# Performance work log

Hardware: AMD Instinct MI355X
Metric: run time of the kernel (lower is better)

## Reference

```python
import jax, jax.numpy as jnp
import numpy as np


def _to_complex(t):
    # last dim 2 = (real, imag) -> complex64
    return jax.lax.complex(t[..., 0], t[..., 1])


def setup_inputs() -> dict:
    key = jax.random.key(0)
    k1, k2, k3, k4 = jax.random.split(key, 4)
    N, C_out, C_in, H, Wf = 2, 64, 3, 256, 129  # Wf = 256//2 + 1 (rfft width)
    X = jax.random.normal(k1, (N, 1, C_in, H, Wf, 2), dtype=jnp.float32)
    D = jax.random.normal(k2, (N, C_out, C_in, H, Wf, 2), dtype=jnp.float32)
    Y = jax.random.normal(k3, (N, C_out, 1, H, Wf, 2), dtype=jnp.float32)
    # alpha is a positive penalty weight; offset away from 0 to avoid blow-up in Z/alpha
    alpha = jax.random.uniform(k4, (N, 1, 1, 1), dtype=jnp.float32) + 0.5
    x_size = np.array([256, 256], dtype=np.int64)  # spatial size for irfft2
    return {"X": X, "D": D, "Y": Y, "alpha": alpha, "x_size": x_size}


def reference(X, D, Y, alpha, x_size):
    C_in = X.shape[2]
    Xc = _to_complex(X)  # (N,1,C_in,H,Wf)
    Dc = _to_complex(D)  # (N,C_out,C_in,H,Wf)
    Yc = _to_complex(Y)  # (N,C_out,1,H,Wf)
    # alpha.unsqueeze(-1).unsqueeze(-1)/C_in: in complex repr one extra axis suffices
    a = (alpha / C_in)[..., None]  # (N,1,1,1,1), real, broadcasts over (N,C_out,C_in,H,Wf)
    Dconj = jnp.conj(Dc)
    Z = Yc * Dc + a * Xc  # (N,C_out,C_in,H,Wf)
    factor1 = Z / a
    numerator = jnp.sum(Dconj * Z, axis=2, keepdims=True)  # (N,C_out,1,H,Wf)
    # csum adds a real scalar (alpha^2) to the real part only
    denominator = a * jnp.sum(Dconj * Dc, axis=2, keepdims=True) + a ** 2
    factor2 = Dc * (numerator / denominator)  # (N,C_out,C_in,H,Wf)
    Xhat = jnp.mean(factor1 - factor2, axis=1)  # (N,C_in,H,Wf)
    Hs, Ws = int(x_size[0]), int(x_size[1])
    # torch.irfft(signal_ndim=2, normalized=False) == full (1/n-normalized) inverse rfft2
    return jnp.fft.irfftn(Xhat, s=(Hs, Ws), axes=(-2, -1))
```

## Files before the change

### kernel.cpp

```cpp
#include <hip/hip_runtime.h>
#include <math.h>

#define H_   256
#define Wf_  129
#define HWf_ 33024
#define CIN_ 3
#define COUT_ 64
#define TW_  0.0245436926f

typedef float f32x4 __attribute__((ext_vector_type(4)));

__global__ __launch_bounds__(256) void solve_stage1(
    const float* __restrict__ X, const float* __restrict__ D,
    const float* __restrict__ Y, const float* __restrict__ alpha,
    float* __restrict__ Xhat)
{
    const int tid  = threadIdx.x;
    const int pl   = tid & 15;
    const int cog  = tid >> 4;
    const int pair = blockIdx.x * 16 + pl;
    const int pos0 = pair * 2;
    const int n    = pos0 / HWf_;
    const int hw0  = pos0 - n * HWf_;

    const float a    = alpha[n] * (1.0f / 3.0f);
    const float inva = 1.0f / a;
    const float a2   = a * a;

    f32x4 x[3];
#pragma unroll
    for (int ci = 0; ci < 3; ++ci)
        x[ci] = *(const f32x4*)(X + ((size_t)(n * 3 + ci) * HWf_ + hw0) * 2);

    const int co0 = cog * 4;
    const float* Dp = D + ((size_t)(n * 64 + co0) * 3) * (HWf_ * 2) + hw0 * 2;
    const float* Yp = Y + ((size_t)(n * 64 + co0)) * (HWf_ * 2) + hw0 * 2;

    float acc[12];
#pragma unroll
    for (int q = 0; q < 12; ++q) acc[q] = 0.f;

#pragma unroll
    for (int co = 0; co < 4; ++co) {
        f32x4 y  = __builtin_nontemporal_load(
                       (const f32x4*)(Yp + (size_t)co * (HWf_ * 2)));
        f32x4 d0 = __builtin_nontemporal_load(
                       (const f32x4*)(Dp + (size_t)(co * 3 + 0) * (HWf_ * 2)));
        f32x4 d1 = __builtin_nontemporal_load(
                       (const f32x4*)(Dp + (size_t)(co * 3 + 1) * (HWf_ * 2)));
        f32x4 d2 = __builtin_nontemporal_load(
                       (const f32x4*)(Dp + (size_t)(co * 3 + 2) * (HWf_ * 2)));

        {
            float s2 = d0[0]*d0[0] + d0[1]*d0[1] + d1[0]*d1[0] + d1[1]*d1[1]
                     + d2[0]*d2[0] + d2[1]*d2[1];
            float sr = d0[0]*x[0][0] + d0[1]*x[0][1] + d1[0]*x[1][0] + d1[1]*x[1][1]
                     + d2[0]*x[2][0] + d2[1]*x[2][1];
            float si = d0[0]*x[0][1] - d0[1]*x[0][0] + d1[0]*x[1][1] - d1[1]*x[1][0]
                     + d2[0]*x[2][1] - d2[1]*x[2][0];
            float nr = y[0] * s2 + a * sr, ni = y[1] * s2 + a * si;
            float invden = 1.0f / (a * s2 + a2);
            float tr = y[0] * inva - nr * invden;
            float ti = y[1] * inva - ni * invden;
            acc[0] += d0[0]*tr - d0[1]*ti;  acc[1] += d0[0]*ti + d0[1]*tr;
            acc[2] += d1[0]*tr - d1[1]*ti;  acc[3] += d1[0]*ti + d1[1]*tr;
            acc[4] += d2[0]*tr - d2[1]*ti;  acc[5] += d2[0]*ti + d2[1]*tr;
        }
        {
            float s2 = d0[2]*d0[2] + d0[3]*d0[3] + d1[2]*d1[2] + d1[3]*d1[3]
                     + d2[2]*d2[2] + d2[3]*d2[3];
            float sr = d0[2]*x[0][2] + d0[3]*x[0][3] + d1[2]*x[1][2] + d1[3]*x[1][3]
                     + d2[2]*x[2][2] + d2[3]*x[2][3];
            float si = d0[2]*x[0][3] - d0[3]*x[0][2] + d1[2]*x[1][3] - d1[3]*x[1][2]
                     + d2[2]*x[2][3] - d2[3]*x[2][2];
            float nr = y[2] * s2 + a * sr, ni = y[3] * s2 + a * si;
            float invden = 1.0f / (a * s2 + a2);
            float tr = y[2] * inva - nr * invden;
            float ti = y[3] * inva - ni * invden;
            acc[6]  += d0[2]*tr - d0[3]*ti;  acc[7]  += d0[2]*ti + d0[3]*tr;
            acc[8]  += d1[2]*tr - d1[3]*ti;  acc[9]  += d1[2]*ti + d1[3]*tr;
            acc[10] += d2[2]*tr - d2[3]*ti;  acc[11] += d2[2]*ti + d2[3]*tr;
        }
    }

    __shared__ float red[16 * 192];
    {
        const int base = cog * 192 + pl * 12;
#pragma unroll
        for (int q = 0; q < 12; ++q) red[base + q] = acc[q];
    }
    __syncthreads();

    if (tid < 192) {
        float s = 0.f;
#pragma unroll
        for (int c = 0; c < 16; ++c) s += red[c * 192 + tid];
        const int P   = tid / 12;
        const int r   = tid - P * 12;
        const int pos = r / 6;
        const int rr  = r - pos * 6;
        const int ci  = rr >> 1;
        const int cc  = rr & 1;
        const int gp  = (blockIdx.x * 16 + P) * 2 + pos;
        const int hw  = gp - n * HWf_;
        const size_t o = ((size_t)(n * 3 + ci) * HWf_ + hw) * 2 + cc;
        Xhat[o] = X[o] + s * (1.0f / 64.0f);
    }
}

__global__ __launch_bounds__(128) void solve_stage2(
    const float2* __restrict__ in, float2* __restrict__ out)
{
    __shared__ float2 col[256];

    const int b    = blockIdx.x;
    const int n_ci = b / Wf_;
    const int w    = b - n_ci * Wf_;
    const int t    = threadIdx.x;

    const float2* src = in + (size_t)n_ci * HWf_ + w;
    col[t]       = src[t * Wf_];
    col[t + 128] = src[(t + 128) * Wf_];
    __syncthreads();

    float wc, wsn;
    sincosf((float)t * TW_, &wsn, &wc);

    float ar = 0.f, ai = 0.f, br = 0.f, bi = 0.f;
    for (int kb = 0; kb < 8; ++kb) {
        const int k0 = kb * 32;
        float tr, ti;
        {
            const int m = (t * k0) & 255;
            float s, c; sincosf((float)m * TW_, &s, &c);
            tr = c; ti = s;
        }
#pragma unroll
        for (int j = 0; j < 32; ++j) {
            const float2 v = col[k0 + j];
            const float pr = v.x * tr - v.y * ti;
            const float pi = v.x * ti + v.y * tr;
            ar += pr; ai += pi;
            if ((k0 + j) & 1) { br -= pr; bi -= pi; }
            else             { br += pr; bi += pi; }
            const float nt = tr * wc - ti * wsn;
            ti = tr * wsn + ti * wc;
            tr = nt;
        }
    }

    float2* dst = out + (size_t)n_ci * HWf_ + w;
    dst[t * Wf_]         = make_float2(ar * (1.0f / 256.0f), ai * (1.0f / 256.0f));
    dst[(t + 128) * Wf_] = make_float2(br * (1.0f / 256.0f), bi * (1.0f / 256.0f));
}

__global__ __launch_bounds__(128) void solve_stage3(
    const float2* __restrict__ in, float* __restrict__ out)
{
    __shared__ float2 row[Wf_];

    const int b = blockIdx.x;
    const int t = threadIdx.x;

    row[t] = in[(size_t)b * Wf_ + t];
    if (t == 0) row[128] = in[(size_t)b * Wf_ + 128];
    __syncthreads();

    float wc, wsn;
    sincosf((float)t * TW_, &wsn, &wc);

    float sa = 0.f, sb = 0.f;
    for (int kb = 0; kb < 4; ++kb) {
        const int k0 = kb * 32;
        float tr, ti;
        {
            const int m = (t * k0) & 255;
            float s, c; sincosf((float)m * TW_, &s, &c);
            tr = c; ti = s;
        }
#pragma unroll
        for (int j = 0; j < 32; ++j) {
            const float2 v = row[k0 + j];
            const float pr = v.x * tr - v.y * ti;
            sa += pr;
            if ((k0 + j) & 1) sb -= pr; else sb += pr;
            const float nt = tr * wc - ti * wsn;
            ti = tr * wsn + ti * wc;
            tr = nt;
        }
    }

    const float sgn  = (t & 1) ? -1.0f : 1.0f;
    const float base = -0.5f * row[0].x + sgn * 0.5f * row[128].x;
    out[(size_t)b * 256 + t]       = (sa + base) * (1.0f / 128.0f);
    out[(size_t)b * 256 + t + 128] = (sb + base) * (1.0f / 128.0f);
}

extern "C" void kernel_launch(void* const* d_in, const int* in_sizes, int n_in,
                              void* d_out, int out_size, void* d_ws, size_t ws_size,
                              hipStream_t stream) {
    const float* X     = (const float*)d_in[0];
    const float* D     = (const float*)d_in[1];
    const float* Y     = (const float*)d_in[2];
    const float* alpha = (const float*)d_in[3];

    float* ws1 = (float*)d_ws;
    float2* ws2 = (float2*)(ws1 + (size_t)CIN_ * 2 * HWf_ * 2);

    solve_stage1<<<2064, 256, 0, stream>>>(X, D, Y, alpha, ws1);
    solve_stage2<<<2 * CIN_ * Wf_, 128, 0, stream>>>((const float2*)ws1, ws2);
    solve_stage3<<<2 * CIN_ * H_, 128, 0, stream>>>(ws2, (float*)d_out);
}
```

Before: 204.2 us.

## Remap stage1 to 64-lane position groups and batch D/Y loads per thread

Stage 1 now assigns 64 consecutive position pairs per block, so a wavefront reads one contiguous 1 KB span per D/Y row instead of 256 B. Each thread covers 16 output channels, and loads for four channels are issued together before any arithmetic, to keep more memory requests in flight. The shared-memory reduction is padded to a stride of 13 to avoid bank conflicts and sums 4 partials instead of 16. The grid shrinks to 516 blocks, so there are far fewer resident waves per CU, and latency hiding depends more on per-thread memory-level parallelism.

```diff
diff --git a/kernel.cpp b/kernel.cpp
--- a/kernel.cpp
+++ b/kernel.cpp
@@ -16,9 +16,9 @@
     float* __restrict__ Xhat)
 {
     const int tid  = threadIdx.x;
-    const int pl   = tid & 15;
-    const int cog  = tid >> 4;
-    const int pair = blockIdx.x * 16 + pl;
+    const int lane = tid & 63;
+    const int cog  = tid >> 6;
+    const int pair = blockIdx.x * 64 + lane;
     const int pos0 = pair * 2;
     const int n    = pos0 / HWf_;
     const int hw0  = pos0 - n * HWf_;
@@ -32,7 +32,7 @@
     for (int ci = 0; ci < 3; ++ci)
         x[ci] = *(const f32x4*)(X + ((size_t)(n * 3 + ci) * HWf_ + hw0) * 2);
 
-    const int co0 = cog * 4;
+    const int co0 = cog * 16;
     const float* Dp = D + ((size_t)(n * 64 + co0) * 3) * (HWf_ * 2) + hw0 * 2;
     const float* Yp = Y + ((size_t)(n * 64 + co0)) * (HWf_ * 2) + hw0 * 2;
 
@@ -40,71 +40,82 @@
 #pragma unroll
     for (int q = 0; q < 12; ++q) acc[q] = 0.f;
 
-#pragma unroll
-    for (int co = 0; co < 4; ++co) {
-        f32x4 y  = __builtin_nontemporal_load(
-                       (const f32x4*)(Yp + (size_t)co * (HWf_ * 2)));
-        f32x4 d0 = __builtin_nontemporal_load(
-                       (const f32x4*)(Dp + (size_t)(co * 3 + 0) * (HWf_ * 2)));
-        f32x4 d1 = __builtin_nontemporal_load(
-                       (const f32x4*)(Dp + (size_t)(co * 3 + 1) * (HWf_ * 2)));
-        f32x4 d2 = __builtin_nontemporal_load(
-                       (const f32x4*)(Dp + (size_t)(co * 3 + 2) * (HWf_ * 2)));
-
-        {
-            float s2 = d0[0]*d0[0] + d0[1]*d0[1] + d1[0]*d1[0] + d1[1]*d1[1]
-                     + d2[0]*d2[0] + d2[1]*d2[1];
-            float sr = d0[0]*x[0][0] + d0[1]*x[0][1] + d1[0]*x[1][0] + d1[1]*x[1][1]
-                     + d2[0]*x[2][0] + d2[1]*x[2][1];
-            float si = d0[0]*x[0][1] - d0[1]*x[0][0] + d1[0]*x[1][1] - d1[1]*x[1][0]
-                     + d2[0]*x[2][1] - d2[1]*x[2][0];
-            float nr = y[0] * s2 + a * sr, ni = y[1] * s2 + a * si;
-            float invden = 1.0f / (a * s2 + a2);
-            float tr = y[0] * inva - nr * invden;
-            float ti = y[1] * inva - ni * invden;
-            acc[0] += d0[0]*tr - d0[1]*ti;  acc[1] += d0[0]*ti + d0[1]*tr;
-            acc[2] += d1[0]*tr - d1[1]*ti;  acc[3] += d1[0]*ti + d1[1]*tr;
-            acc[4] += d2[0]*tr - d2[1]*ti;  acc[5] += d2[0]*ti + d2[1]*tr;
-        }
-        {
-            float s2 = d0[2]*d0[2] + d0[3]*d0[3] + d1[2]*d1[2] + d1[3]*d1[3]
-                     + d2[2]*d2[2] + d2[3]*d2[3];
-            float sr = d0[2]*x[0][2] + d0[3]*x[0][3] + d1[2]*x[1][2] + d1[3]*x[1][3]
-                     + d2[2]*x[2][2] + d2[3]*x[2][3];
-            float si = d0[2]*x[0][3] - d0[3]*x[0][2] + d1[2]*x[1][3] - d1[3]*x[1][2]
-                     + d2[2]*x[2][3] - d2[3]*x[2][2];
-            float nr = y[2] * s2 + a * sr, ni = y[3] * s2 + a * si;
-            float invden = 1.0f / (a * s2 + a2);
-            float tr = y[2] * inva - nr * invden;
-            float ti = y[3] * inva - ni * invden;
-            acc[6]  += d0[2]*tr - d0[3]*ti;  acc[7]  += d0[2]*ti + d0[3]*tr;
-            acc[8]  += d1[2]*tr - d1[3]*ti;  acc[9]  += d1[2]*ti + d1[3]*tr;
-            acc[10] += d2[2]*tr - d2[3]*ti;  acc[11] += d2[2]*ti + d2[3]*tr;
-        }
-    }
-
-    __shared__ float red[16 * 192];
+    for (int cb = 0; cb < 4; ++cb) {
+        f32x4 yv[4], dv[12];
+#pragma unroll
+        for (int j = 0; j < 4; ++j) {
+            const int co = cb * 4 + j;
+            yv[j]        = __builtin_nontemporal_load(
+                               (const f32x4*)(Yp + (size_t)co * (HWf_ * 2)));
+            dv[j*3 + 0]  = __builtin_nontemporal_load(
+                               (const f32x4*)(Dp + (size_t)(co*3 + 0) * (HWf_ * 2)));
+            dv[j*3 + 1]  = __builtin_nontemporal_load(
+                               (const f32x4*)(Dp + (size_t)(co*3 + 1) * (HWf_ * 2)));
+            dv[j*3 + 2]  = __builtin_nontemporal_load(
+                               (const f32x4*)(Dp + (size_t)(co*3 + 2) * (HWf_ * 2)));
+        }
+#pragma unroll
+        for (int j = 0; j < 4; ++j) {
+            const f32x4 y  = yv[j];
+            const f32x4 d0 = dv[j*3 + 0];
+            const f32x4 d1 = dv[j*3 + 1];
+            const f32x4 d2 = dv[j*3 + 2];
+            {
+                float s2 = d0[0]*d0[0] + d0[1]*d0[1] + d1[0]*d1[0] + d1[1]*d1[1]
+                         + d2[0]*d2[0] + d2[1]*d2[1];
+                float sr = d0[0]*x[0][0] + d0[1]*x[0][1] + d1[0]*x[1][0] + d1[1]*x[1][1]
+                         + d2[0]*x[2][0] + d2[1]*x[2][1];
+                float si = d0[0]*x[0][1] - d0[1]*x[0][0] + d1[0]*x[1][1] - d1[1]*x[1][0]
+                         + d2[0]*x[2][1] - d2[1]*x[2][0];
+                float nr = y[0] * s2 + a * sr, ni = y[1] * s2 + a * si;
+                float invden = 1.0f / (a * s2 + a2);
+                float tr = y[0] * inva - nr * invden;
+                float ti = y[1] * inva - ni * invden;
+                acc[0] += d0[0]*tr - d0[1]*ti;  acc[1] += d0[0]*ti + d0[1]*tr;
+                acc[2] += d1[0]*tr - d1[1]*ti;  acc[3] += d1[0]*ti + d1[1]*tr;
+                acc[4] += d2[0]*tr - d2[1]*ti;  acc[5] += d2[0]*ti + d2[1]*tr;
+            }
+            {
+                float s2 = d0[2]*d0[2] + d0[3]*d0[3] + d1[2]*d1[2] + d1[3]*d1[3]
+                         + d2[2]*d2[2] + d2[3]*d2[3];
+                float sr = d0[2]*x[0][2] + d0[3]*x[0][3] + d1[2]*x[1][2] + d1[3]*x[1][3]
+                         + d2[2]*x[2][2] + d2[3]*x[2][3];
+                float si = d0[2]*x[0][3] - d0[3]*x[0][2] + d1[2]*x[1][3] - d1[3]*x[1][2]
+                         + d2[2]*x[2][3] - d2[3]*x[2][2];
+                float nr = y[2] * s2 + a * sr, ni = y[3] * s2 + a * si;
+                float invden = 1.0f / (a * s2 + a2);
+                float tr = y[2] * inva - nr * invden;
+                float ti = y[3] * inva - ni * invden;
+                acc[6]  += d0[2]*tr - d0[3]*ti;  acc[7]  += d0[2]*ti + d0[3]*tr;
+                acc[8]  += d1[2]*tr - d1[3]*ti;  acc[9]  += d1[2]*ti + d1[3]*tr;
+                acc[10] += d2[2]*tr - d2[3]*ti;  acc[11] += d2[2]*ti + d2[3]*tr;
+            }
+        }
+    }
+
+    __shared__ float red[4 * 832];
     {
-        const int base = cog * 192 + pl * 12;
+        const int base = cog * 832 + lane * 13;
 #pragma unroll
         for (int q = 0; q < 12; ++q) red[base + q] = acc[q];
     }
     __syncthreads();
 
-    if (tid < 192) {
-        float s = 0.f;
-#pragma unroll
-        for (int c = 0; c < 16; ++c) s += red[c * 192 + tid];
-        const int P   = tid / 12;
-        const int r   = tid - P * 12;
+#pragma unroll
+    for (int it = 0; it < 3; ++it) {
+        const int o = tid + 256 * it;
+        const int P = o / 12;
+        const int r = o - P * 12;
+        const int idx = P * 13 + r;
+        const float s = red[idx] + red[832 + idx] + red[1664 + idx] + red[2496 + idx];
         const int pos = r / 6;
         const int rr  = r - pos * 6;
         const int ci  = rr >> 1;
         const int cc  = rr & 1;
-        const int gp  = (blockIdx.x * 16 + P) * 2 + pos;
+        const int gp  = (blockIdx.x * 64 + P) * 2 + pos;
         const int hw  = gp - n * HWf_;
-        const size_t o = ((size_t)(n * 3 + ci) * HWf_ + hw) * 2 + cc;
-        Xhat[o] = X[o] + s * (1.0f / 64.0f);
+        const size_t oa = ((size_t)(n * 3 + ci) * HWf_ + hw) * 2 + cc;
+        Xhat[oa] = X[oa] + s * (1.0f / 64.0f);
     }
 }
 
@@ -207,7 +218,7 @@
     float* ws1 = (float*)d_ws;
     float2* ws2 = (float2*)(ws1 + (size_t)CIN_ * 2 * HWf_ * 2);
 
-    solve_stage1<<<2064, 256, 0, stream>>>(X, D, Y, alpha, ws1);
+    solve_stage1<<<516, 256, 0, stream>>>(X, D, Y, alpha, ws1);
     solve_stage2<<<2 * CIN_ * Wf_, 128, 0, stream>>>((const float2*)ws1, ws2);
     solve_stage3<<<2 * CIN_ * H_, 128, 0, stream>>>(ws2, (float*)d_out);
 }
```

Result: slower. 218.6 us (+7.1%).
